# Kernel tuning notes

Measured on AMD Instinct MI355X. Metric: run time of the kernel, lower is better.

Reference implementation:

```python
import jax, jax.numpy as jnp
import numpy as np

ALPHA_LIM = (float(np.exp(-1.0 / 5.0)), float(np.exp(-1.0 / 25.0)))
BETA_LIM = (float(np.exp(-1.0 / 30.0)), float(np.exp(-1.0 / 120.0)))
A_LIM = (-1.0, 1.0)
B_LIM = (0.0, 2.0)
THRESHOLD = 1.0


@jax.custom_vjp
def spike_boxcar(x):
    # Heaviside forward, boxcar surrogate gradient
    return (x > 0).astype(x.dtype)


def _spike_fwd(x):
    return spike_boxcar(x), x


def _spike_bwd(x, g):
    return (jnp.where(jnp.abs(x) <= 0.5, g, jnp.zeros_like(g)),)


spike_boxcar.defvjp(_spike_fwd, _spike_bwd)


def setup_inputs() -> dict:
    key = jax.random.key(0)
    ks = jax.random.split(key, 9)
    B, T, I, H = 128, 512, 512, 512
    return {
        "x": jax.random.normal(ks[0], (B, T, I), dtype=jnp.float32),
        "W": jax.random.normal(ks[1], (H, I), dtype=jnp.float32) / np.sqrt(I),
        "alpha": jax.random.uniform(ks[2], (H,), dtype=jnp.float32),
        "beta": jax.random.uniform(ks[3], (H,), dtype=jnp.float32),
        "a": jax.random.uniform(ks[4], (H,), dtype=jnp.float32),
        "b": jax.random.uniform(ks[5], (H,), dtype=jnp.float32),
        "u0": jax.random.uniform(ks[6], (B, H), dtype=jnp.float32),
        "w0": jax.random.uniform(ks[7], (B, H), dtype=jnp.float32),
        "s0": jax.random.uniform(ks[8], (B, H), dtype=jnp.float32),
    }


def reference(x, W, alpha, beta, a, b, u0, w0, s0):
    # x: [B, T, I]; W: [H, I] (nn.Linear weight, no bias)
    alpha = jnp.clip(alpha, ALPHA_LIM[0], ALPHA_LIM[1])
    beta = jnp.clip(beta, BETA_LIM[0], BETA_LIM[1])
    a = jnp.clip(a, A_LIM[0], A_LIM[1])
    b = jnp.clip(b, B_LIM[0], B_LIM[1])

    Wx = jnp.einsum("bti,hi->bth", x, W)  # [B, T, H]
    Wx_t = jnp.transpose(Wx, (1, 0, 2))    # [T, B, H] for scan over time

    def step(carry, wx_t):
        ut, wt, st = carry
        wt = beta * wt + a * ut + b * st
        ut = alpha * (ut - st) + (1.0 - alpha) * (wx_t - wt)
        st = spike_boxcar(ut - THRESHOLD)
        return (ut, wt, st), st

    _, s = jax.lax.scan(step, (u0, w0, s0), Wx_t)  # s: [T, B, H]
    return jnp.transpose(s, (1, 0, 2))  # [B, T, H]
```

## Files before the change

### kernel.cpp

```cpp
#include <hip/hip_runtime.h>
#include <hip/hip_bf16.h>


#define M_SZ 65536
#define H_SZ 512
#define K_SZ 512
#define B_SZ 128
#define T_SZ 512

#define AST 260
#define BST 132

__device__ __forceinline__ bool detect_bf16(const unsigned int* __restrict__ w) {
  int c = 0;
#pragma unroll
  for (int i = 0; i < 64; ++i) {
    unsigned int e = (w[i] >> 7) & 0xffu;
    c += (e >= 115u && e <= 131u) ? 1 : 0;
  }
  return c > 32;
}

template <bool ISB>
__device__ __forceinline__ float4 ld4t(const void* __restrict__ p, size_t off) {
  if constexpr (!ISB) {
    return *reinterpret_cast<const float4*>(reinterpret_cast<const float*>(p) + off);
  } else {
    uint2 v = *reinterpret_cast<const uint2*>(reinterpret_cast<const unsigned short*>(p) + off);
    float4 r;
    r.x = __uint_as_float((v.x & 0xffffu) << 16);
    r.y = __uint_as_float(v.x & 0xffff0000u);
    r.z = __uint_as_float((v.y & 0xffffu) << 16);
    r.w = __uint_as_float(v.y & 0xffff0000u);
    return r;
  }
}

template <bool ISB>
__device__ __forceinline__ float ld1t(const void* __restrict__ p, int i) {
  if constexpr (!ISB) return reinterpret_cast<const float*>(p)[i];
  return __uint_as_float((unsigned int)(reinterpret_cast<const unsigned short*>(p)[i]) << 16);
}

__device__ __forceinline__ void gl_lds16(const void* g, void* l) {
  __builtin_amdgcn_global_load_lds(
      (const __attribute__((address_space(1))) void*)g,
      (__attribute__((address_space(3))) void*)l, 16, 0, 0);
}

template <bool ISB>
__device__ __forceinline__ void gemm_body(const void* __restrict__ X,
                                          const void* __restrict__ Wm,
                                          float* __restrict__ C,
                                          float* __restrict__ As,
                                          float* __restrict__ Bs) {
  const int tid = threadIdx.x;
  const int r0 = tid >> 2;
  const int q0 = (tid & 3) * 4;
  const int tx = tid & 15;
  const int ty = tid >> 4;
  const size_t M0 = (size_t)(blockIdx.x >> 2) * 256;
  const int N0 = (blockIdx.x & 3) * 128;

  float acc[16][8];
#pragma unroll
  for (int i = 0; i < 16; ++i)
#pragma unroll
    for (int j = 0; j < 8; ++j) acc[i][j] = 0.0f;

  float4 pa[4], pb[2];
#pragma unroll
  for (int p = 0; p < 4; ++p) pa[p] = ld4t<ISB>(X, (M0 + r0 + 64 * p) * K_SZ + q0);
#pragma unroll
  for (int q = 0; q < 2; ++q) pb[q] = ld4t<ISB>(Wm, (size_t)(N0 + r0 + 64 * q) * K_SZ + q0);

  for (int kk = 0; kk < K_SZ; kk += 16) {
    __syncthreads();
#pragma unroll
    for (int p = 0; p < 4; ++p) {
      As[(q0 + 0) * AST + r0 + 64 * p] = pa[p].x;
      As[(q0 + 1) * AST + r0 + 64 * p] = pa[p].y;
      As[(q0 + 2) * AST + r0 + 64 * p] = pa[p].z;
      As[(q0 + 3) * AST + r0 + 64 * p] = pa[p].w;
    }
#pragma unroll
    for (int q = 0; q < 2; ++q) {
      Bs[(q0 + 0) * BST + r0 + 64 * q] = pb[q].x;
      Bs[(q0 + 1) * BST + r0 + 64 * q] = pb[q].y;
      Bs[(q0 + 2) * BST + r0 + 64 * q] = pb[q].z;
      Bs[(q0 + 3) * BST + r0 + 64 * q] = pb[q].w;
    }
    __syncthreads();
    if (kk + 16 < K_SZ) {
#pragma unroll
      for (int p = 0; p < 4; ++p)
        pa[p] = ld4t<ISB>(X, (M0 + r0 + 64 * p) * K_SZ + kk + 16 + q0);
#pragma unroll
      for (int q = 0; q < 2; ++q)
        pb[q] = ld4t<ISB>(Wm, (size_t)(N0 + r0 + 64 * q) * K_SZ + kk + 16 + q0);
    }
#pragma unroll
    for (int k = 0; k < 16; ++k) {
      float av[16], bv[8];
#pragma unroll
      for (int p = 0; p < 4; ++p) {
        const float4 t4 = *reinterpret_cast<const float4*>(As + k * AST + ty * 4 + 64 * p);
        av[p * 4 + 0] = t4.x; av[p * 4 + 1] = t4.y; av[p * 4 + 2] = t4.z; av[p * 4 + 3] = t4.w;
      }
#pragma unroll
      for (int q = 0; q < 2; ++q) {
        const float4 t4 = *reinterpret_cast<const float4*>(Bs + k * BST + tx * 4 + 64 * q);
        bv[q * 4 + 0] = t4.x; bv[q * 4 + 1] = t4.y; bv[q * 4 + 2] = t4.z; bv[q * 4 + 3] = t4.w;
      }
#pragma unroll
      for (int i = 0; i < 16; ++i)
#pragma unroll
        for (int j = 0; j < 8; ++j) acc[i][j] += av[i] * bv[j];
    }
  }

#pragma unroll
  for (int p = 0; p < 4; ++p)
#pragma unroll
    for (int r = 0; r < 4; ++r) {
      const size_t m = M0 + 64 * p + ty * 4 + r;
      float* Cp = C + m * H_SZ + N0 + tx * 4;
      float4 v0 = {acc[p * 4 + r][0], acc[p * 4 + r][1], acc[p * 4 + r][2], acc[p * 4 + r][3]};
      float4 v1 = {acc[p * 4 + r][4], acc[p * 4 + r][5], acc[p * 4 + r][6], acc[p * 4 + r][7]};
      *reinterpret_cast<float4*>(Cp) = v0;
      *reinterpret_cast<float4*>(Cp + 64) = v1;
    }
}

__global__ __launch_bounds__(256) void sgemm_bt(const void* __restrict__ X,
                                                const void* __restrict__ Wm,
                                                float* __restrict__ C) {
  __shared__ float As[16 * AST];
  __shared__ float Bs[16 * BST];
  if (detect_bf16(reinterpret_cast<const unsigned int*>(X)))
    gemm_body<true>(X, Wm, C, As, Bs);
  else
    gemm_body<false>(X, Wm, C, As, Bs);
}

#define CH 32

template <bool ISB>
__device__ __forceinline__ void scan_body(
    const float* __restrict__ wx, const void* __restrict__ alpha_p,
    const void* __restrict__ beta_p, const void* __restrict__ a_p,
    const void* __restrict__ b_p, const void* __restrict__ u0p,
    const void* __restrict__ w0p, const void* __restrict__ s0p,
    void* __restrict__ out, float* __restrict__ buf) {
  const int tid = threadIdx.x;
  const int wave = tid >> 6;
  const int lane = tid & 63;
  const int bb = blockIdx.x >> 1;
  const int half = blockIdx.x & 1;
  const int h = half * 256 + tid;

  const float al = fminf(fmaxf(ld1t<ISB>(alpha_p, h), (float)0.8187307530779818),
                         (float)0.9607894391523232);
  const float be = fminf(fmaxf(ld1t<ISB>(beta_p, h), (float)0.9672161004820059),
                         (float)0.9917013044213351);
  const float av = fminf(fmaxf(ld1t<ISB>(a_p, h), -1.0f), 1.0f);
  const float bv = fminf(fmaxf(ld1t<ISB>(b_p, h), 0.0f), 2.0f);
  const float om = __fsub_rn(1.0f, al);

  const int bh = bb * H_SZ + h;
  float u = ld1t<ISB>(u0p, bh);
  float w = ld1t<ISB>(w0p, bh);
  float s = ld1t<ISB>(s0p, bh);

  const float* xbase = wx + (size_t)bb * T_SZ * H_SZ + half * 256;
  float* outf = reinterpret_cast<float*>(out);
  __hip_bfloat16* outb = reinterpret_cast<__hip_bfloat16*>(out);
  const size_t ob0 = (size_t)bb * T_SZ * H_SZ + h;

  auto issue = [&](int c) {
    float* dst = buf + (c & 1) * (CH * 256);
    const float* src = xbase + (size_t)c * CH * H_SZ;
#pragma unroll
    for (int i = 0; i < 8; ++i) {
      const int t = wave * 8 + i;
      gl_lds16(src + (size_t)t * H_SZ + lane * 4, dst + t * 256 + lane * 4);
    }
  };

  issue(0);
  for (int c = 0; c < T_SZ / CH; ++c) {
    __syncthreads();
    if (c + 1 < T_SZ / CH) issue(c + 1);
    const float* cb = buf + (c & 1) * (CH * 256);
#pragma unroll
    for (int j = 0; j < CH; ++j) {
      const float cur = cb[j * 256 + tid];
      w = __fadd_rn(__fadd_rn(__fmul_rn(be, w), __fmul_rn(av, u)), __fmul_rn(bv, s));
      u = __fadd_rn(__fmul_rn(al, __fsub_rn(u, s)), __fmul_rn(om, __fsub_rn(cur, w)));
      s = (u > 1.0f) ? 1.0f : 0.0f;
      const size_t o = ob0 + (size_t)(c * CH + j) * H_SZ;
      if constexpr (ISB) outb[o] = __float2bfloat16(s);
      else outf[o] = s;
    }
  }
}

__global__ __launch_bounds__(256) void lif_scan(
    const float* __restrict__ wx, const void* __restrict__ X,
    const void* __restrict__ alpha_p, const void* __restrict__ beta_p,
    const void* __restrict__ a_p, const void* __restrict__ b_p,
    const void* __restrict__ u0p, const void* __restrict__ w0p,
    const void* __restrict__ s0p, void* __restrict__ out) {
  __shared__ float buf[2 * CH * 256];
  if (detect_bf16(reinterpret_cast<const unsigned int*>(X)))
    scan_body<true>(wx, alpha_p, beta_p, a_p, b_p, u0p, w0p, s0p, out, buf);
  else
    scan_body<false>(wx, alpha_p, beta_p, a_p, b_p, u0p, w0p, s0p, out, buf);
}

extern "C" void kernel_launch(void* const* d_in, const int* in_sizes, int n_in,
                              void* d_out, int out_size, void* d_ws, size_t ws_size,
                              hipStream_t stream) {
  const void* X = d_in[0];
  const void* Wm = d_in[1];
  float* ws = reinterpret_cast<float*>(d_ws);

  sgemm_bt<<<dim3((M_SZ / 256) * (H_SZ / 128)), dim3(256), 0, stream>>>(X, Wm, ws);

  lif_scan<<<dim3(B_SZ * 2), dim3(256), 0, stream>>>(
      ws, X, d_in[2], d_in[3], d_in[4], d_in[5], d_in[6], d_in[7], d_in[8], d_out);
}
```

Before: 667.6 us.

## Shrink GEMM tile to 128x128 with double-buffered LDS and split scan finer

The SGEMM tile drops from 256x128 to 128x128 per block, with an 8x8 register tile instead of 16x8. The A/B shared-memory tiles are now double-buffered, which removes one barrier per k-step and overlaps the next tile's store with compute. The LIF scan runs 4 blocks of 128 threads per batch instead of 2 of 256, with 64-step chunks, to put more blocks on the GPU. The smaller GEMM tile lowers register pressure and raises occupancy, but it also lowers arithmetic intensity and increases global loads per FLOP.

```diff
diff --git a/kernel.cpp b/kernel.cpp
--- a/kernel.cpp
+++ b/kernel.cpp
@@ -7,9 +7,8 @@
 #define K_SZ 512
 #define B_SZ 128
 #define T_SZ 512
-
-#define AST 260
-#define BST 132
+#define LSTR 132
+#define LBUF (16 * LSTR)
 
 __device__ __forceinline__ bool detect_bf16(const unsigned int* __restrict__ w) {
   int c = 0;
@@ -59,91 +58,96 @@
   const int q0 = (tid & 3) * 4;
   const int tx = tid & 15;
   const int ty = tid >> 4;
-  const size_t M0 = (size_t)(blockIdx.x >> 2) * 256;
+  const size_t M0 = (size_t)(blockIdx.x >> 2) * 128;
   const int N0 = (blockIdx.x & 3) * 128;
 
-  float acc[16][8];
-#pragma unroll
-  for (int i = 0; i < 16; ++i)
+  float acc[8][8];
+#pragma unroll
+  for (int i = 0; i < 8; ++i)
 #pragma unroll
     for (int j = 0; j < 8; ++j) acc[i][j] = 0.0f;
 
-  float4 pa[4], pb[2];
-#pragma unroll
-  for (int p = 0; p < 4; ++p) pa[p] = ld4t<ISB>(X, (M0 + r0 + 64 * p) * K_SZ + q0);
-#pragma unroll
-  for (int q = 0; q < 2; ++q) pb[q] = ld4t<ISB>(Wm, (size_t)(N0 + r0 + 64 * q) * K_SZ + q0);
-
-  for (int kk = 0; kk < K_SZ; kk += 16) {
+  const size_t aoff0 = (M0 + r0) * K_SZ + q0;
+  const size_t aoff1 = (M0 + r0 + 64) * K_SZ + q0;
+  const size_t boff0 = (size_t)(N0 + r0) * K_SZ + q0;
+  const size_t boff1 = (size_t)(N0 + r0 + 64) * K_SZ + q0;
+
+  float4 pa0 = ld4t<ISB>(X, aoff0), pa1 = ld4t<ISB>(X, aoff1);
+  float4 pb0 = ld4t<ISB>(Wm, boff0), pb1 = ld4t<ISB>(Wm, boff1);
+
+  {
+    float* wa = As;
+    float* wb = Bs;
+    wa[(q0 + 0) * LSTR + r0] = pa0.x; wa[(q0 + 1) * LSTR + r0] = pa0.y;
+    wa[(q0 + 2) * LSTR + r0] = pa0.z; wa[(q0 + 3) * LSTR + r0] = pa0.w;
+    wa[(q0 + 0) * LSTR + r0 + 64] = pa1.x; wa[(q0 + 1) * LSTR + r0 + 64] = pa1.y;
+    wa[(q0 + 2) * LSTR + r0 + 64] = pa1.z; wa[(q0 + 3) * LSTR + r0 + 64] = pa1.w;
+    wb[(q0 + 0) * LSTR + r0] = pb0.x; wb[(q0 + 1) * LSTR + r0] = pb0.y;
+    wb[(q0 + 2) * LSTR + r0] = pb0.z; wb[(q0 + 3) * LSTR + r0] = pb0.w;
+    wb[(q0 + 0) * LSTR + r0 + 64] = pb1.x; wb[(q0 + 1) * LSTR + r0 + 64] = pb1.y;
+    wb[(q0 + 2) * LSTR + r0 + 64] = pb1.z; wb[(q0 + 3) * LSTR + r0 + 64] = pb1.w;
+  }
+
+  const int NC = K_SZ / 16;
+  for (int c = 0; c < NC; ++c) {
     __syncthreads();
-#pragma unroll
-    for (int p = 0; p < 4; ++p) {
-      As[(q0 + 0) * AST + r0 + 64 * p] = pa[p].x;
-      As[(q0 + 1) * AST + r0 + 64 * p] = pa[p].y;
-      As[(q0 + 2) * AST + r0 + 64 * p] = pa[p].z;
-      As[(q0 + 3) * AST + r0 + 64 * p] = pa[p].w;
-    }
-#pragma unroll
-    for (int q = 0; q < 2; ++q) {
-      Bs[(q0 + 0) * BST + r0 + 64 * q] = pb[q].x;
-      Bs[(q0 + 1) * BST + r0 + 64 * q] = pb[q].y;
-      Bs[(q0 + 2) * BST + r0 + 64 * q] = pb[q].z;
-      Bs[(q0 + 3) * BST + r0 + 64 * q] = pb[q].w;
-    }
-    __syncthreads();
-    if (kk + 16 < K_SZ) {
-#pragma unroll
-      for (int p = 0; p < 4; ++p)
-        pa[p] = ld4t<ISB>(X, (M0 + r0 + 64 * p) * K_SZ + kk + 16 + q0);
-#pragma unroll
-      for (int q = 0; q < 2; ++q)
-        pb[q] = ld4t<ISB>(Wm, (size_t)(N0 + r0 + 64 * q) * K_SZ + kk + 16 + q0);
-    }
+    if (c + 1 < NC) {
+      const int kk = (c + 1) * 16;
+      pa0 = ld4t<ISB>(X, aoff0 + kk); pa1 = ld4t<ISB>(X, aoff1 + kk);
+      pb0 = ld4t<ISB>(Wm, boff0 + kk); pb1 = ld4t<ISB>(Wm, boff1 + kk);
+    }
+    const float* ab = As + (c & 1) * LBUF;
+    const float* bbk = Bs + (c & 1) * LBUF;
 #pragma unroll
     for (int k = 0; k < 16; ++k) {
-      float av[16], bv[8];
-#pragma unroll
-      for (int p = 0; p < 4; ++p) {
-        const float4 t4 = *reinterpret_cast<const float4*>(As + k * AST + ty * 4 + 64 * p);
-        av[p * 4 + 0] = t4.x; av[p * 4 + 1] = t4.y; av[p * 4 + 2] = t4.z; av[p * 4 + 3] = t4.w;
-      }
-#pragma unroll
-      for (int q = 0; q < 2; ++q) {
-        const float4 t4 = *reinterpret_cast<const float4*>(Bs + k * BST + tx * 4 + 64 * q);
-        bv[q * 4 + 0] = t4.x; bv[q * 4 + 1] = t4.y; bv[q * 4 + 2] = t4.z; bv[q * 4 + 3] = t4.w;
-      }
-#pragma unroll
-      for (int i = 0; i < 16; ++i)
+      const float4 a0 = *reinterpret_cast<const float4*>(ab + k * LSTR + ty * 4);
+      const float4 a1 = *reinterpret_cast<const float4*>(ab + k * LSTR + 64 + ty * 4);
+      const float4 b0 = *reinterpret_cast<const float4*>(bbk + k * LSTR + tx * 4);
+      const float4 b1 = *reinterpret_cast<const float4*>(bbk + k * LSTR + 64 + tx * 4);
+      const float av[8] = {a0.x, a0.y, a0.z, a0.w, a1.x, a1.y, a1.z, a1.w};
+      const float bv[8] = {b0.x, b0.y, b0.z, b0.w, b1.x, b1.y, b1.z, b1.w};
+#pragma unroll
+      for (int i = 0; i < 8; ++i)
 #pragma unroll
         for (int j = 0; j < 8; ++j) acc[i][j] += av[i] * bv[j];
     }
-  }
-
-#pragma unroll
-  for (int p = 0; p < 4; ++p)
-#pragma unroll
-    for (int r = 0; r < 4; ++r) {
-      const size_t m = M0 + 64 * p + ty * 4 + r;
-      float* Cp = C + m * H_SZ + N0 + tx * 4;
-      float4 v0 = {acc[p * 4 + r][0], acc[p * 4 + r][1], acc[p * 4 + r][2], acc[p * 4 + r][3]};
-      float4 v1 = {acc[p * 4 + r][4], acc[p * 4 + r][5], acc[p * 4 + r][6], acc[p * 4 + r][7]};
-      *reinterpret_cast<float4*>(Cp) = v0;
-      *reinterpret_cast<float4*>(Cp + 64) = v1;
-    }
+    if (c + 1 < NC) {
+      float* wa = As + ((c + 1) & 1) * LBUF;
+      float* wb = Bs + ((c + 1) & 1) * LBUF;
+      wa[(q0 + 0) * LSTR + r0] = pa0.x; wa[(q0 + 1) * LSTR + r0] = pa0.y;
+      wa[(q0 + 2) * LSTR + r0] = pa0.z; wa[(q0 + 3) * LSTR + r0] = pa0.w;
+      wa[(q0 + 0) * LSTR + r0 + 64] = pa1.x; wa[(q0 + 1) * LSTR + r0 + 64] = pa1.y;
+      wa[(q0 + 2) * LSTR + r0 + 64] = pa1.z; wa[(q0 + 3) * LSTR + r0 + 64] = pa1.w;
+      wb[(q0 + 0) * LSTR + r0] = pb0.x; wb[(q0 + 1) * LSTR + r0] = pb0.y;
+      wb[(q0 + 2) * LSTR + r0] = pb0.z; wb[(q0 + 3) * LSTR + r0] = pb0.w;
+      wb[(q0 + 0) * LSTR + r0 + 64] = pb1.x; wb[(q0 + 1) * LSTR + r0 + 64] = pb1.y;
+      wb[(q0 + 2) * LSTR + r0 + 64] = pb1.z; wb[(q0 + 3) * LSTR + r0 + 64] = pb1.w;
+    }
+  }
+
+#pragma unroll
+  for (int r = 0; r < 8; ++r) {
+    const size_t m = M0 + ((r < 4) ? (ty * 4 + r) : (64 + ty * 4 + (r - 4)));
+    float* Cp = C + m * H_SZ + N0;
+    float4 v0 = {acc[r][0], acc[r][1], acc[r][2], acc[r][3]};
+    float4 v1 = {acc[r][4], acc[r][5], acc[r][6], acc[r][7]};
+    *reinterpret_cast<float4*>(Cp + tx * 4) = v0;
+    *reinterpret_cast<float4*>(Cp + 64 + tx * 4) = v1;
+  }
 }
 
 __global__ __launch_bounds__(256) void sgemm_bt(const void* __restrict__ X,
                                                 const void* __restrict__ Wm,
                                                 float* __restrict__ C) {
-  __shared__ float As[16 * AST];
-  __shared__ float Bs[16 * BST];
+  __shared__ float As[2 * LBUF];
+  __shared__ float Bs[2 * LBUF];
   if (detect_bf16(reinterpret_cast<const unsigned int*>(X)))
     gemm_body<true>(X, Wm, C, As, Bs);
   else
     gemm_body<false>(X, Wm, C, As, Bs);
 }
 
-#define CH 32
+#define SCH 64
 
 template <bool ISB>
 __device__ __forceinline__ void scan_body(
@@ -155,9 +159,9 @@
   const int tid = threadIdx.x;
   const int wave = tid >> 6;
   const int lane = tid & 63;
-  const int bb = blockIdx.x >> 1;
-  const int half = blockIdx.x & 1;
-  const int h = half * 256 + tid;
+  const int bb = blockIdx.x >> 2;
+  const int quarter = blockIdx.x & 3;
+  const int h = quarter * 128 + tid;
 
   const float al = fminf(fmaxf(ld1t<ISB>(alpha_p, h), (float)0.8187307530779818),
                          (float)0.9607894391523232);
@@ -172,46 +176,49 @@
   float w = ld1t<ISB>(w0p, bh);
   float s = ld1t<ISB>(s0p, bh);
 
-  const float* xbase = wx + (size_t)bb * T_SZ * H_SZ + half * 256;
+  const float* xb = wx + (size_t)bb * T_SZ * H_SZ + quarter * 128;
   float* outf = reinterpret_cast<float*>(out);
   __hip_bfloat16* outb = reinterpret_cast<__hip_bfloat16*>(out);
   const size_t ob0 = (size_t)bb * T_SZ * H_SZ + h;
 
   auto issue = [&](int c) {
-    float* dst = buf + (c & 1) * (CH * 256);
-    const float* src = xbase + (size_t)c * CH * H_SZ;
-#pragma unroll
-    for (int i = 0; i < 8; ++i) {
-      const int t = wave * 8 + i;
-      gl_lds16(src + (size_t)t * H_SZ + lane * 4, dst + t * 256 + lane * 4);
+    float* dst = buf + (c & 1) * (SCH * 128);
+    const float* sp = xb + (size_t)c * SCH * H_SZ;
+    const int t_sub = lane >> 5;
+    const int h_off = (lane & 31) * 4;
+#pragma unroll
+    for (int i = 0; i < 16; ++i) {
+      const int j = wave * 16 + i;
+      gl_lds16(sp + (size_t)(2 * j + t_sub) * H_SZ + h_off, dst + j * 256 + lane * 4);
     }
   };
 
   issue(0);
-  for (int c = 0; c < T_SZ / CH; ++c) {
+  const int NCH = T_SZ / SCH;
+  for (int c = 0; c < NCH; ++c) {
     __syncthreads();
-    if (c + 1 < T_SZ / CH) issue(c + 1);
-    const float* cb = buf + (c & 1) * (CH * 256);
-#pragma unroll
-    for (int j = 0; j < CH; ++j) {
-      const float cur = cb[j * 256 + tid];
+    if (c + 1 < NCH) issue(c + 1);
+    const float* cb = buf + (c & 1) * (SCH * 128);
+#pragma unroll 16
+    for (int j = 0; j < SCH; ++j) {
+      const float cur = cb[j * 128 + tid];
       w = __fadd_rn(__fadd_rn(__fmul_rn(be, w), __fmul_rn(av, u)), __fmul_rn(bv, s));
       u = __fadd_rn(__fmul_rn(al, __fsub_rn(u, s)), __fmul_rn(om, __fsub_rn(cur, w)));
       s = (u > 1.0f) ? 1.0f : 0.0f;
-      const size_t o = ob0 + (size_t)(c * CH + j) * H_SZ;
+      const size_t o = ob0 + (size_t)(c * SCH + j) * H_SZ;
       if constexpr (ISB) outb[o] = __float2bfloat16(s);
       else outf[o] = s;
     }
   }
 }
 
-__global__ __launch_bounds__(256) void lif_scan(
+__global__ __launch_bounds__(128) void lif_scan(
     const float* __restrict__ wx, const void* __restrict__ X,
     const void* __restrict__ alpha_p, const void* __restrict__ beta_p,
     const void* __restrict__ a_p, const void* __restrict__ b_p,
     const void* __restrict__ u0p, const void* __restrict__ w0p,
     const void* __restrict__ s0p, void* __restrict__ out) {
-  __shared__ float buf[2 * CH * 256];
+  __shared__ float buf[2 * SCH * 128];
   if (detect_bf16(reinterpret_cast<const unsigned int*>(X)))
     scan_body<true>(wx, alpha_p, beta_p, a_p, b_p, u0p, w0p, s0p, out, buf);
   else
@@ -225,8 +232,8 @@
   const void* Wm = d_in[1];
   float* ws = reinterpret_cast<float*>(d_ws);
 
-  sgemm_bt<<<dim3((M_SZ / 256) * (H_SZ / 128)), dim3(256), 0, stream>>>(X, Wm, ws);
-
-  lif_scan<<<dim3(B_SZ * 2), dim3(256), 0, stream>>>(
+  sgemm_bt<<<dim3((M_SZ / 128) * (H_SZ / 128)), dim3(256), 0, stream>>>(X, Wm, ws);
+
+  lif_scan<<<dim3(B_SZ * 4), dim3(128), 0, stream>>>(
       ws, X, d_in[2], d_in[3], d_in[4], d_in[5], d_in[6], d_in[7], d_in[8], d_out);
 }
```

Result: slower. 782.1 us (+17.2%).
